# Kernel optimization log

Measured on AMD Instinct MI355X. Metric: run time of the kernel, lower is better.

## Reference

```python
import jax, jax.numpy as jnp
import numpy as np

N_NODES = 50000
N_EDGES = 1600000
IN_FEATS = 128
ENC_H = 20
DEC_H = 64


def setup_inputs() -> dict:
    key = jax.random.key(0)
    ks = jax.random.split(key, 14)
    inp = {}
    inp["x"] = jax.random.normal(ks[0], (N_NODES, IN_FEATS), dtype=jnp.float32)
    inp["edge_index"] = jax.random.randint(ks[1], (2, N_EDGES), 0, N_NODES, dtype=jnp.int64)
    inp["node_id"] = 0
    inp["noise_normal"] = jax.random.normal(ks[2], (N_EDGES, ENC_H), dtype=jnp.float32)
    inp["noise_u"] = jax.random.uniform(ks[3], (N_EDGES, 1), dtype=jnp.float32)
    # parameters (glorot-ish init)
    def lin(k, fan_in, fan_out):
        s = 1.0 / np.sqrt(fan_in)
        return jax.random.uniform(k, (fan_in, fan_out), jnp.float32, -s, s)
    inp["W_gc"] = lin(ks[4], IN_FEATS, ENC_H)
    inp["b_gc"] = jnp.zeros((ENC_H,), jnp.float32)
    inp["W_mu"] = lin(ks[5], 3 * ENC_H, ENC_H)
    inp["b_mu"] = jnp.zeros((ENC_H,), jnp.float32)
    inp["W_var"] = lin(ks[6], 3 * ENC_H, ENC_H)
    inp["b_var"] = jnp.zeros((ENC_H,), jnp.float32)
    inp["W_d1"] = lin(ks[7], ENC_H, DEC_H)
    inp["b_d1"] = jnp.zeros((DEC_H,), jnp.float32)
    inp["W_d2"] = lin(ks[8], DEC_H, 1)
    inp["b_d2"] = jnp.zeros((1,), jnp.float32)
    return inp


def _gcn_conv(x, edge_index, W, b):
    """PyG-style GCNConv: add self-loops, symmetric D^-1/2 (A+I) D^-1/2 norm."""
    n = x.shape[0]
    sl = jnp.arange(n, dtype=edge_index.dtype)
    row = jnp.concatenate([edge_index[0], sl])  # source
    col = jnp.concatenate([edge_index[1], sl])  # target
    xw = x @ W  # [N, H]
    deg = jax.ops.segment_sum(jnp.ones_like(col, dtype=xw.dtype), col, num_segments=n)
    dinv = jnp.where(deg > 0, jax.lax.rsqrt(deg), 0.0)
    norm = dinv[row] * dinv[col]  # [E+N]
    out = jax.ops.segment_sum(xw[row] * norm[:, None], col, num_segments=n)
    return out + b


def reference(x, edge_index, node_id, noise_normal, noise_u,
              W_gc, b_gc, W_mu, b_mu, W_var, b_var, W_d1, b_d1, W_d2, b_d2):
    # GCN encoder
    x1 = jax.nn.relu(_gcn_conv(x, edge_index, W_gc, b_gc))  # [N, H]
    # per-edge concat: [src_embed | dst_embed | node_id_embed]
    rows, cols = edge_index[0], edge_index[1]
    node_embed = jnp.broadcast_to(x1[node_id][None, :], (rows.shape[0], x1.shape[1]))
    x2 = jnp.concatenate([x1[rows], x1[cols], node_embed], axis=1)  # [E, 3H]
    # variational heads + reparameterization
    mu = x2 @ W_mu + b_mu
    sigma = jnp.exp(x2 @ W_var + b_var)
    z = mu + sigma * noise_normal  # [E, H]
    # decoder MLP
    h = jax.nn.relu(z @ W_d1 + b_d1)
    sampling_weights = jax.nn.relu(h @ W_d2 + b_d2)  # [E, 1]
    # gumbel-sigmoid sample (training=True, bias=0.0 -> bias'=1e-4, temperature=1.0)
    bias = 0.0001
    eps = (bias - (1.0 - bias)) * noise_u + (1.0 - bias)
    gate = jnp.log(eps) - jnp.log(1.0 - eps) + sampling_weights
    return jax.nn.sigmoid(gate)
```

## Files before the change

kernel.cpp:

```cpp
#include <hip/hip_runtime.h>

#define NFEAT 128
#define H 20
#define DH 64
#define SCAN_T 1024
#define BE 64
#define NB 192
#define HW 12800

typedef __attribute__((ext_vector_type(8))) short short8;
typedef __attribute__((ext_vector_type(4))) float f32x4;

__device__ __forceinline__ unsigned short f2bf(float f) {
    union { float f; unsigned u; } v; v.f = f;
    unsigned r = v.u + 0x7fff + ((v.u >> 16) & 1);
    return (unsigned short)(r >> 16);
}
__device__ __forceinline__ unsigned pk2(unsigned short a, unsigned short b) {
    return (unsigned)a | ((unsigned)b << 16);
}
__device__ __forceinline__ float bfel(uint4 v, int j) {
    unsigned word = (j < 2) ? v.x : (j < 4) ? v.y : (j < 6) ? v.z : v.w;
    unsigned u = (j & 1) ? (word & 0xFFFF0000u) : (word << 16);
    return __int_as_float((int)u);
}

template <int CTRL>
__device__ __forceinline__ float dpp_add(float x) {
    int y = __builtin_amdgcn_update_dpp(0, __float_as_int(x), CTRL, 0xF, 0xF, true);
    return x + __int_as_float(y);
}
__device__ __forceinline__ float sum16(float x) {
    x = dpp_add<0xB1>(x);
    x = dpp_add<0x4E>(x);
    x = dpp_add<0x124>(x);
    x = dpp_add<0x128>(x);
    return x;
}

__global__ __launch_bounds__(256) void k_prep(const float* __restrict__ Wd1,
                                              unsigned short* __restrict__ Bd1,
                                              int* __restrict__ deg, int* __restrict__ csum,
                                              float* __restrict__ bcat2, int N) {
    int t = blockIdx.x * blockDim.x + threadIdx.x;
    if (t < N) deg[t] = 0;
    if (t < 256) csum[t] = 0;
    if (t < 64) bcat2[t] = 0.f;
    if (t < 256) {
        int f = t >> 6, l = t & 63;
        int n = f * 16 + (l & 15);
#pragma unroll
        for (int j = 0; j < 8; j++) {
            int k = (l >> 4) * 8 + j;
            float v = (k < H) ? Wd1[k * DH + n] : 0.f;
            Bd1[(size_t)f * 512 + l * 8 + j] = f2bf(v);
        }
    }
}

__global__ __launch_bounds__(512) void k_hist(const int* __restrict__ cols,
                                              unsigned* __restrict__ hist, int* __restrict__ csum,
                                              int E, int N) {
    __shared__ unsigned h[HW];
    __shared__ int cs[256];
    int wstride = (N + 3) >> 2;
    int nchunks = (N + 255) >> 8;
    for (int i = threadIdx.x; i < wstride; i += 512) h[i] = 0;
    if (threadIdx.x < 256) cs[threadIdx.x] = 0;
    __syncthreads();
    int chunk = (E + NB - 1) / NB;
    int beg = blockIdx.x * chunk, end = min(beg + chunk, E);
    for (int i = beg + threadIdx.x; i < end; i += 512) {
        int c = __builtin_nontemporal_load(cols + i);
        atomicAdd(&h[c >> 2], 1u << ((c & 3) * 8));
    }
    __syncthreads();
    unsigned* dst = hist + (size_t)blockIdx.x * wstride;
    for (int i = threadIdx.x; i < wstride; i += 512) {
        unsigned w = h[i];
        dst[i] = w;
        if (w) {
            int s = (w & 0xFF) + ((w >> 8) & 0xFF) + ((w >> 16) & 0xFF) + (w >> 24);
            atomicAdd(&cs[i >> 6], s);
        }
    }
    __syncthreads();
    for (int j = threadIdx.x; j < nchunks; j += 512)
        if (cs[j]) atomicAdd(&csum[j], cs[j]);
}

__global__ __launch_bounds__(256) void k_scansmall(const int* __restrict__ chunkSum,
                                                   int* __restrict__ chunkOff, int nb) {
    __shared__ int sc[256];
    int t = threadIdx.x;
    int v0 = (t < nb) ? chunkSum[t] : 0;
    sc[t] = v0;
    __syncthreads();
    for (int off = 1; off < 256; off <<= 1) {
        int v = (t >= off) ? sc[t - off] : 0;
        __syncthreads();
        sc[t] += v;
        __syncthreads();
    }
    if (t < nb) chunkOff[t] = sc[t] - v0;
}

__global__ __launch_bounds__(256) void k_bases(const unsigned* __restrict__ hist,
                                               const int* __restrict__ chunkOff,
                                               unsigned char* __restrict__ delta,
                                               int* __restrict__ offsets, int* __restrict__ deg,
                                               int N, int E) {
    __shared__ int sc[256];
    int c = blockIdx.x * 256 + threadIdx.x;
    int wstride = (N + 3) >> 2;
    int sh = (c & 3) * 8;
    bool valid = c < N;
    int cw = valid ? (c >> 2) : 0;
    unsigned cnt[NB / 4];
    int d = 0;
#pragma unroll
    for (int b = 0; b < NB; b++) {
        unsigned w = hist[(size_t)b * wstride + cw];
        unsigned byte = (w >> sh) & 0xFF;
        if ((b & 3) == 0) cnt[b >> 2] = byte;
        else cnt[b >> 2] |= byte << ((b & 3) * 8);
        d += (int)byte;
    }
    if (!valid) d = 0;
    sc[threadIdx.x] = d;
    __syncthreads();
    for (int off = 1; off < 256; off <<= 1) {
        int v = (threadIdx.x >= off) ? sc[threadIdx.x - off] : 0;
        __syncthreads();
        sc[threadIdx.x] += v;
        __syncthreads();
    }
    if (valid) {
        int base = chunkOff[blockIdx.x] + sc[threadIdx.x] - d;
        offsets[c] = base;
        deg[c] = d;
        int run = 0;
#pragma unroll
        for (int b = 0; b < NB; b++) {
            delta[(size_t)b * N + c] = (unsigned char)run;
            run += (int)((cnt[b >> 2] >> ((b & 3) * 8)) & 0xFF);
        }
    }
    if (blockIdx.x == 0 && threadIdx.x == 0) offsets[N] = E;
}

__global__ __launch_bounds__(512) void k_place(const int* __restrict__ rows, const int* __restrict__ cols,
                                               const int* __restrict__ offsets,
                                               const unsigned char* __restrict__ delta,
                                               unsigned short* __restrict__ srcs, int E, int N) {
    __shared__ unsigned h[HW];
    int wstride = (N + 3) >> 2;
    for (int i = threadIdx.x; i < wstride; i += 512) h[i] = 0;
    __syncthreads();
    int chunk = (E + NB - 1) / NB;
    int beg = blockIdx.x * chunk, end = min(beg + chunk, E);
    const unsigned char* mydelta = delta + (size_t)blockIdx.x * N;
    for (int i = beg + threadIdx.x; i < end; i += 512) {
        int c = __builtin_nontemporal_load(cols + i);
        int r = __builtin_nontemporal_load(rows + i);
        int sh = (c & 3) * 8;
        unsigned old = atomicAdd(&h[c >> 2], 1u << sh);
        int rank = (old >> sh) & 0xFF;
        int pos = offsets[c] + (int)mydelta[c] + rank;
        srcs[pos] = (unsigned short)r;
    }
}

__global__ __launch_bounds__(256) void k_deg(const int* __restrict__ cols, int* __restrict__ deg, int E) {
    int t = blockIdx.x * blockDim.x + threadIdx.x;
    if (t < E) atomicAdd(&deg[cols[t]], 1);
}

__global__ __launch_bounds__(SCAN_T) void k_scan(const int* __restrict__ deg, int* __restrict__ offsets,
                                                 int* __restrict__ cursor, int N) {
    __shared__ int sums[SCAN_T];
    int t = threadIdx.x;
    int chunk = (N + SCAN_T - 1) / SCAN_T;
    int beg = t * chunk;
    int end = min(beg + chunk, N);
    int s = 0;
    for (int i = beg; i < end; i++) s += deg[i];
    sums[t] = s;
    __syncthreads();
    for (int off = 1; off < SCAN_T; off <<= 1) {
        int v = (t >= off) ? sums[t - off] : 0;
        __syncthreads();
        sums[t] += v;
        __syncthreads();
    }
    int run = (t == 0) ? 0 : sums[t - 1];
    for (int i = beg; i < end; i++) {
        offsets[i] = run;
        cursor[i] = run;
        run += deg[i];
    }
    if (t == SCAN_T - 1) offsets[N] = sums[SCAN_T - 1];
}

__global__ __launch_bounds__(256) void k_bucket_csr(const int* __restrict__ rows, const int* __restrict__ cols,
                                                    int* __restrict__ cursor, int* __restrict__ srcs, int E) {
    int e = blockIdx.x * blockDim.x + threadIdx.x;
    if (e >= E) return;
    int pos = atomicAdd(&cursor[cols[e]], 1);
    srcs[pos] = rows[e];
}

__global__ __launch_bounds__(256) void k_xw_xs(const float* __restrict__ x, const float* __restrict__ Wgc,
                                               const int* __restrict__ deg,
                                               float* __restrict__ xs, int N) {
    __shared__ float Ws[NFEAT * H];
    for (int i = threadIdx.x; i < NFEAT * H; i += blockDim.x) Ws[i] = Wgc[i];
    __syncthreads();
    int n = blockIdx.x * blockDim.x + threadIdx.x;
    if (n >= N) return;
    float acc[H];
#pragma unroll
    for (int j = 0; j < H; j++) acc[j] = 0.f;
    const float4* x4 = (const float4*)(x + (size_t)n * NFEAT);
#pragma unroll 4
    for (int k4 = 0; k4 < NFEAT / 4; k4++) {
        float4 xv = x4[k4];
#pragma unroll
        for (int s = 0; s < 4; s++) {
            float xk = (s == 0) ? xv.x : (s == 1) ? xv.y : (s == 2) ? xv.z : xv.w;
            const float4* wrow = (const float4*)(Ws + (k4 * 4 + s) * H);
#pragma unroll
            for (int q = 0; q < 5; q++) {
                float4 w = wrow[q];
                acc[q * 4 + 0] += xk * w.x;
                acc[q * 4 + 1] += xk * w.y;
                acc[q * 4 + 2] += xk * w.z;
                acc[q * 4 + 3] += xk * w.w;
            }
        }
    }
    float di = rsqrtf((float)(deg[n] + 1));
    float4* o = (float4*)(xs + (size_t)n * H);
#pragma unroll
    for (int q = 0; q < 5; q++)
        o[q] = make_float4(acc[q * 4 + 0] * di, acc[q * 4 + 1] * di, acc[q * 4 + 2] * di, acc[q * 4 + 3] * di);
}

template <typename IT>
__device__ __forceinline__ void gather_core16(const float* __restrict__ xs, const IT* __restrict__ idx,
                                              int beg, int end, int n, int sl, int degn,
                                              const float* __restrict__ bgc,
                                              unsigned short* __restrict__ PAo, unsigned short* __restrict__ PBo,
                                              int nid, const float* __restrict__ Wmu, const float* __restrict__ Wvar,
                                              const float* __restrict__ bmu, const float* __restrict__ bvar,
                                              float* __restrict__ bcat2) {
    float acc[H];
    if (sl == 0) {
        const float4* self = (const float4*)(xs + (size_t)n * H);
#pragma unroll
        for (int q = 0; q < 5; q++) {
            float4 v = self[q];
            acc[q * 4 + 0] = v.x; acc[q * 4 + 1] = v.y; acc[q * 4 + 2] = v.z; acc[q * 4 + 3] = v.w;
        }
    } else {
#pragma unroll
        for (int j = 0; j < H; j++) acc[j] = 0.f;
    }
#pragma unroll 2
    for (int i = beg + sl; i < end; i += 16) {
        int r = (int)__builtin_nontemporal_load(idx + i);
        const float4* p = (const float4*)(xs + (size_t)r * H);
#pragma unroll
        for (int q = 0; q < 5; q++) {
            float4 v = p[q];
            acc[q * 4 + 0] += v.x; acc[q * 4 + 1] += v.y; acc[q * 4 + 2] += v.z; acc[q * 4 + 3] += v.w;
        }
    }
#pragma unroll
    for (int j = 0; j < H; j++) acc[j] = sum16(acc[j]);
    float di = rsqrtf((float)(degn + 1));
    float x1f[H];
#pragma unroll
    for (int j = 0; j < H; j++) x1f[j] = fmaxf(di * acc[j] + bgc[j], 0.f);

#pragma unroll
    for (int t = 0; t < 6; t++) {
        int v = sl + 16 * t;
        int part = v / 24;
        int j = v - part * 24;
        float s = 0.f;
        if (j < 20) {
            const float* W = (part & 1) ? Wvar : Wmu;
            int k0 = (part < 2) ? 0 : 20;
#pragma unroll
            for (int k = 0; k < H; k++) s += x1f[k] * W[(k0 + k) * H + j];
        }
        unsigned short* T = (part < 2) ? PAo : PBo;
        int off = (j >> 3) * 16 + (part & 1) * 8 + (j & 7);
        T[(size_t)n * 48 + off] = f2bf(s);
    }

    if (n == nid) {
#pragma unroll
        for (int base = 0; base < 48; base += 16) {
            int jj = base + sl;
            if (jj < 40) {
                bool ismu = jj < 20;
                int col = ismu ? jj : jj - 20;
                const float* W = ismu ? Wmu : Wvar;
                float s = ismu ? bmu[col] : bvar[col];
#pragma unroll
                for (int k = 0; k < H; k++) s += x1f[k] * W[(2 * H + k) * H + col];
                bcat2[jj] = s;
            }
        }
    }
}

__global__ __launch_bounds__(256) void k_gather_csr16(const float* __restrict__ xs, const unsigned short* __restrict__ srcs,
                                                      const int* __restrict__ offsets, const int* __restrict__ deg,
                                                      const float* __restrict__ bgc,
                                                      unsigned short* __restrict__ PAo, unsigned short* __restrict__ PBo,
                                                      const int* __restrict__ node_id,
                                                      const float* __restrict__ Wmu, const float* __restrict__ Wvar,
                                                      const float* __restrict__ bmu, const float* __restrict__ bvar,
                                                      float* __restrict__ bcat2, int N) {
    int wave = (blockIdx.x * 256 + threadIdx.x) >> 6;
    int lane = threadIdx.x & 63;
    int n = wave * 4 + (lane >> 4);
    if (n >= N) return;
    gather_core16(xs, srcs, offsets[n], offsets[n + 1], n, lane & 15, deg[n], bgc, PAo, PBo,
                  node_id[0], Wmu, Wvar, bmu, bvar, bcat2);
}

__global__ __launch_bounds__(256) void k_gather_csr(const float* __restrict__ xs, const int* __restrict__ srcs,
                                                    const int* __restrict__ offsets, const int* __restrict__ deg,
                                                    const float* __restrict__ bgc,
                                                    unsigned short* __restrict__ PAo, unsigned short* __restrict__ PBo,
                                                    const int* __restrict__ node_id,
                                                    const float* __restrict__ Wmu, const float* __restrict__ Wvar,
                                                    const float* __restrict__ bmu, const float* __restrict__ bvar,
                                                    float* __restrict__ bcat2, int N) {
    int wave = (blockIdx.x * 256 + threadIdx.x) >> 6;
    int lane = threadIdx.x & 63;
    int n = wave * 4 + (lane >> 4);
    if (n >= N) return;
    gather_core16(xs, srcs, offsets[n], offsets[n + 1], n, lane & 15, deg[n], bgc, PAo, PBo,
                  node_id[0], Wmu, Wvar, bmu, bvar, bcat2);
}

__global__ __launch_bounds__(256) void k_mlp(
    const unsigned short* __restrict__ PA, const unsigned short* __restrict__ PBt,
    const int* __restrict__ rows, const int* __restrict__ cols,
    const float* __restrict__ noise_n, const float* __restrict__ noise_u,
    const unsigned short* __restrict__ Bd1g,
    const float* __restrict__ bcat2, const float* __restrict__ b_d1,
    const float* __restrict__ W_d2, const float* __restrict__ b_d2,
    float* __restrict__ out, int E) {

    int tid = threadIdx.x;
    int e0 = blockIdx.x * BE;
    int l = tid & 63, w = tid >> 6;
    int m = l & 15, quad = l >> 4;

    int ea = e0 + w * 16 + m;
    int ec = (ea < E) ? ea : E - 1;
    int r = rows[ec], c = cols[ec];

    uint4 pam = {0, 0, 0, 0}, pav = {0, 0, 0, 0}, pbm = {0, 0, 0, 0}, pbv = {0, 0, 0, 0};
    float nz[8], bm[8], bv[8];
#pragma unroll
    for (int j = 0; j < 8; j++) { nz[j] = 0.f; bm[j] = 0.f; bv[j] = 0.f; }
    if (quad < 3) {
        const char* pa = (const char*)PA + (size_t)r * 96 + quad * 32;
        const char* pb = (const char*)PBt + (size_t)c * 96 + quad * 32;
        pam = *(const uint4*)pa;  pav = *(const uint4*)(pa + 16);
        pbm = *(const uint4*)pb;  pbv = *(const uint4*)(pb + 16);
        float4 b0 = *(const float4*)(bcat2 + quad * 8);
        float4 b1 = *(const float4*)(bcat2 + quad * 8 + 4);
        bm[0] = b0.x; bm[1] = b0.y; bm[2] = b0.z; bm[3] = b0.w;
        bm[4] = b1.x; bm[5] = b1.y; bm[6] = b1.z; bm[7] = b1.w;
        float4 v0 = *(const float4*)(bcat2 + 20 + quad * 8);
        float4 v1 = *(const float4*)(bcat2 + 20 + quad * 8 + 4);
        bv[0] = v0.x; bv[1] = v0.y; bv[2] = v0.z; bv[3] = v0.w;
        bv[4] = v1.x; bv[5] = v1.y; bv[6] = v1.z; bv[7] = v1.w;
        const float* np = noise_n + (size_t)ec * H + quad * 8;
        float4 n0 = *(const float4*)np;
        nz[0] = n0.x; nz[1] = n0.y; nz[2] = n0.z; nz[3] = n0.w;
        if (quad < 2) {
            float4 n1 = *(const float4*)(np + 4);
            nz[4] = n1.x; nz[5] = n1.y; nz[6] = n1.z; nz[7] = n1.w;
        }
    }

    unsigned zp[4];
#pragma unroll
    for (int jj = 0; jj < 4; jj++) {
        unsigned short zh[2];
#pragma unroll
        for (int h2 = 0; h2 < 2; h2++) {
            int j = jj * 2 + h2;
            float zmu = bfel(pam, j) + bfel(pbm, j) + bm[j];
            float zva = bfel(pav, j) + bfel(pbv, j) + bv[j];
            float z = zmu + __expf(zva) * nz[j];
            z = (quad * 8 + j < 20) ? z : 0.f;
            zh[h2] = f2bf(z);
        }
        zp[jj] = pk2(zh[0], zh[1]);
    }
    union { unsigned u[4]; short8 s; } au;
    au.u[0] = zp[0]; au.u[1] = zp[1]; au.u[2] = zp[2]; au.u[3] = zp[3];
    short8 a2 = au.s;

    float p0 = 0.f, p1 = 0.f, p2 = 0.f, p3 = 0.f;
#pragma unroll
    for (int t4 = 0; t4 < 4; t4++) {
        f32x4 acc = {0.f, 0.f, 0.f, 0.f};
        short8 bb = *(const short8*)(Bd1g + t4 * 512 + l * 8);
        acc = __builtin_amdgcn_mfma_f32_16x16x32_bf16(a2, bb, acc, 0, 0, 0);
        int col = t4 * 16 + m;
        float bias = b_d1[col], wo = W_d2[col];
        p0 += fmaxf(acc[0] + bias, 0.f) * wo;
        p1 += fmaxf(acc[1] + bias, 0.f) * wo;
        p2 += fmaxf(acc[2] + bias, 0.f) * wo;
        p3 += fmaxf(acc[3] + bias, 0.f) * wo;
    }
    p0 = sum16(p0); p1 = sum16(p1); p2 = sum16(p2); p3 = sum16(p3);
    if (m < 4) {
        float swv = (m == 0) ? p0 : (m == 1) ? p1 : (m == 2) ? p2 : p3;
        int e = e0 + w * 16 + quad * 4 + m;
        if (e < E) {
            float sw = fmaxf(swv + b_d2[0], 0.f);
            float u = noise_u[e];
            float ev = 0.9999f - 0.9998f * u;
            float t = __expf(-sw);
            out[e] = ev / (ev + (1.f - ev) * t);
        }
    }
}

extern "C" void kernel_launch(void* const* d_in, const int* in_sizes, int n_in,
                              void* d_out, int out_size, void* d_ws, size_t ws_size,
                              hipStream_t stream) {
    const int N = in_sizes[0] / NFEAT;
    const int E = in_sizes[1] / 2;

    const float* x       = (const float*)d_in[0];
    const int*   ei      = (const int*)d_in[1];
    const int*   rows    = ei;
    const int*   cols    = ei + E;
    const int*   node_id = (const int*)d_in[2];
    const float* noise_n = (const float*)d_in[3];
    const float* noise_u = (const float*)d_in[4];
    const float* Wgc  = (const float*)d_in[5];
    const float* bgc  = (const float*)d_in[6];
    const float* Wmu  = (const float*)d_in[7];
    const float* bmu  = (const float*)d_in[8];
    const float* Wvar = (const float*)d_in[9];
    const float* bvar = (const float*)d_in[10];
    const float* Wd1  = (const float*)d_in[11];
    const float* bd1  = (const float*)d_in[12];
    const float* Wd2  = (const float*)d_in[13];
    const float* bd2  = (const float*)d_in[14];
    float* out = (float*)d_out;

    const int B = 256;
    int gN  = (N + B - 1) / B;
    int gG  = (N + 15) / 16;
    int gE  = (E + B - 1) / B;
    int gM  = (E + BE - 1) / BE;
    int nBins = (N + 255) / 256;

    char* ws = (char*)d_ws;
    size_t wstride   = (size_t)((N + 3) >> 2);
    size_t pa_sz     = (((size_t)N * 96) + 255) & ~255ULL;
    size_t hist_sz   = ((NB * wstride * 4) + 255) & ~255ULL;
    size_t histreg   = (hist_sz > 2 * pa_sz) ? hist_sz : 2 * pa_sz;
    size_t o_deg     = 0;
    size_t o_off     = o_deg  + (((size_t)N * 4 + 255) & ~255ULL);
    size_t o_csum    = o_off  + (((size_t)(N + 1) * 4 + 255) & ~255ULL);
    size_t o_coff    = o_csum + 1024;
    size_t o_hist    = o_coff + 1024;
    size_t o_delta   = o_hist  + histreg;
    size_t o_srcs    = o_delta + (((size_t)NB * N + 255) & ~255ULL);
    size_t o_xs      = o_srcs  + (((size_t)E * 2 + 255) & ~255ULL);
    size_t o_Bd1     = o_xs    + (((size_t)N * H * 4 + 255) & ~255ULL);
    size_t o_bcat2   = o_Bd1   + 4096;
    size_t need      = o_bcat2 + 256;

    bool main_path = (ws_size >= need) && (N <= 4 * HW) && (N < 65536) && (nBins <= 256);

    if (main_path) {
        int*   deg     = (int*)(ws + o_deg);
        int*   offsets = (int*)(ws + o_off);
        int*   csum    = (int*)(ws + o_csum);
        int*   coff    = (int*)(ws + o_coff);
        unsigned* hist = (unsigned*)(ws + o_hist);
        unsigned short* PA = (unsigned short*)(ws + o_hist);
        unsigned short* PB = (unsigned short*)(ws + o_hist + pa_sz);
        unsigned char* delta = (unsigned char*)(ws + o_delta);
        unsigned short* srcs = (unsigned short*)(ws + o_srcs);
        float* xs      = (float*)(ws + o_xs);
        unsigned short* Bd1  = (unsigned short*)(ws + o_Bd1);
        float* bcat2   = (float*)(ws + o_bcat2);

        k_prep<<<gN, B, 0, stream>>>(Wd1, Bd1, deg, csum, bcat2, N);
        k_hist<<<NB, 512, 0, stream>>>(cols, hist, csum, E, N);
        k_scansmall<<<1, B, 0, stream>>>(csum, coff, nBins);
        k_bases<<<nBins, B, 0, stream>>>(hist, coff, delta, offsets, deg, N, E);
        k_xw_xs<<<gN, B, 0, stream>>>(x, Wgc, deg, xs, N);
        k_place<<<NB, 512, 0, stream>>>(rows, cols, offsets, delta, srcs, E, N);
        k_gather_csr16<<<gG, B, 0, stream>>>(xs, srcs, offsets, deg, bgc, PA, PB,
                                             node_id, Wmu, Wvar, bmu, bvar, bcat2, N);
        k_mlp<<<gM, B, 0, stream>>>(PA, PB, rows, cols, noise_n, noise_u,
                                    Bd1, bcat2, bd1, Wd2, bd2, out, E);
    } else {
        size_t f_deg   = 0;
        size_t f_off   = f_deg + (((size_t)N * 4 + 255) & ~255ULL);
        size_t f_cur   = f_off + (((size_t)(N + 1) * 4 + 255) & ~255ULL);
        size_t f_srcs  = f_cur + (((size_t)N * 4 + 255) & ~255ULL);
        size_t f_xs    = f_srcs + (((size_t)E * 4 + 255) & ~255ULL);
        size_t f_PA    = f_xs + (((size_t)N * H * 4 + 255) & ~255ULL);
        size_t f_PB    = f_PA + pa_sz;
        size_t f_Bd1   = f_PB + pa_sz;
        size_t f_bcat2 = f_Bd1 + 4096;

        int*   deg     = (int*)(ws + f_deg);
        int*   offsets = (int*)(ws + f_off);
        int*   cursor  = (int*)(ws + f_cur);
        int*   srcs    = (int*)(ws + f_srcs);
        float* xs      = (float*)(ws + f_xs);
        unsigned short* PA = (unsigned short*)(ws + f_PA);
        unsigned short* PB = (unsigned short*)(ws + f_PB);
        unsigned short* Bd1 = (unsigned short*)(ws + f_Bd1);
        float* bcat2   = (float*)(ws + f_bcat2);

        k_prep<<<gN, B, 0, stream>>>(Wd1, Bd1, deg, cursor, bcat2, N);
        k_deg<<<gE, B, 0, stream>>>(cols, deg, E);
        k_scan<<<1, SCAN_T, 0, stream>>>(deg, offsets, cursor, N);
        k_bucket_csr<<<gE, B, 0, stream>>>(rows, cols, cursor, srcs, E);
        k_xw_xs<<<gN, B, 0, stream>>>(x, Wgc, deg, xs, N);
        k_gather_csr<<<gG, B, 0, stream>>>(xs, srcs, offsets, deg, bgc, PA, PB,
                                           node_id, Wmu, Wvar, bmu, bvar, bcat2, N);
        k_mlp<<<gM, B, 0, stream>>>(PA, PB, rows, cols, noise_n, noise_u,
                                    Bd1, bcat2, bd1, Wd2, bd2, out, E);
    }
}
```

Before: 431.2 us.

## Record ranks in histogram, flatten placement, compact PA/PB rows, two edge tiles per MLP wave

The histogram kernel now stores each edge's within-block rank, so the placement kernel becomes a flat one-thread-per-edge scatter and no longer needs a second LDS atomic pass with 192 large blocks. The per-node PA/PB bf16 rows shrink from 96 to 80 bytes by packing the last four mu/var features tightly, which cuts gather traffic in the MLP. The MLP kernel processes 128 edges per block, two 16-edge MFMA tiles per wave, to amortise bias and weight loads and raise memory-level parallelism. This costs an extra E-byte rank array write and read, plus more registers per thread in the MLP.

```diff
diff --git a/kernel.cpp b/kernel.cpp
--- a/kernel.cpp
+++ b/kernel.cpp
@@ -4,7 +4,7 @@
 #define H 20
 #define DH 64
 #define SCAN_T 1024
-#define BE 64
+#define BE2 128
 #define NB 192
 #define HW 12800
 
@@ -45,7 +45,7 @@
     int t = blockIdx.x * blockDim.x + threadIdx.x;
     if (t < N) deg[t] = 0;
     if (t < 256) csum[t] = 0;
-    if (t < 64) bcat2[t] = 0.f;
+    if (t < 128) bcat2[t] = 0.f;
     if (t < 256) {
         int f = t >> 6, l = t & 63;
         int n = f * 16 + (l & 15);
@@ -60,6 +60,7 @@
 
 __global__ __launch_bounds__(512) void k_hist(const int* __restrict__ cols,
                                               unsigned* __restrict__ hist, int* __restrict__ csum,
+                                              unsigned char* __restrict__ rank,
                                               int E, int N) {
     __shared__ unsigned h[HW];
     __shared__ int cs[256];
@@ -72,7 +73,9 @@
     int beg = blockIdx.x * chunk, end = min(beg + chunk, E);
     for (int i = beg + threadIdx.x; i < end; i += 512) {
         int c = __builtin_nontemporal_load(cols + i);
-        atomicAdd(&h[c >> 2], 1u << ((c & 3) * 8));
+        int sh = (c & 3) * 8;
+        unsigned old = atomicAdd(&h[c >> 2], 1u << sh);
+        rank[i] = (unsigned char)((old >> sh) & 0xFF);
     }
     __syncthreads();
     unsigned* dst = hist + (size_t)blockIdx.x * wstride;
@@ -149,26 +152,18 @@
     if (blockIdx.x == 0 && threadIdx.x == 0) offsets[N] = E;
 }
 
-__global__ __launch_bounds__(512) void k_place(const int* __restrict__ rows, const int* __restrict__ cols,
+__global__ __launch_bounds__(256) void k_place(const int* __restrict__ rows, const int* __restrict__ cols,
                                                const int* __restrict__ offsets,
                                                const unsigned char* __restrict__ delta,
-                                               unsigned short* __restrict__ srcs, int E, int N) {
-    __shared__ unsigned h[HW];
-    int wstride = (N + 3) >> 2;
-    for (int i = threadIdx.x; i < wstride; i += 512) h[i] = 0;
-    __syncthreads();
-    int chunk = (E + NB - 1) / NB;
-    int beg = blockIdx.x * chunk, end = min(beg + chunk, E);
-    const unsigned char* mydelta = delta + (size_t)blockIdx.x * N;
-    for (int i = beg + threadIdx.x; i < end; i += 512) {
-        int c = __builtin_nontemporal_load(cols + i);
-        int r = __builtin_nontemporal_load(rows + i);
-        int sh = (c & 3) * 8;
-        unsigned old = atomicAdd(&h[c >> 2], 1u << sh);
-        int rank = (old >> sh) & 0xFF;
-        int pos = offsets[c] + (int)mydelta[c] + rank;
-        srcs[pos] = (unsigned short)r;
-    }
+                                               const unsigned char* __restrict__ rank,
+                                               unsigned short* __restrict__ srcs, int E, int N, int chunk) {
+    int e = blockIdx.x * 256 + threadIdx.x;
+    if (e >= E) return;
+    int c = cols[e];
+    int r = rows[e];
+    int b = e / chunk;
+    int pos = offsets[c] + (int)delta[(size_t)b * N + c] + (int)rank[e];
+    srcs[pos] = (unsigned short)r;
 }
 
 __global__ __launch_bounds__(256) void k_deg(const int* __restrict__ cols, int* __restrict__ deg, int E) {
@@ -284,20 +279,19 @@
     for (int j = 0; j < H; j++) x1f[j] = fmaxf(di * acc[j] + bgc[j], 0.f);
 
 #pragma unroll
-    for (int t = 0; t < 6; t++) {
+    for (int t = 0; t < 5; t++) {
         int v = sl + 16 * t;
-        int part = v / 24;
-        int j = v - part * 24;
+        int part = v / 20;
+        int j = v - part * 20;
+        const float* W = (part & 1) ? Wvar : Wmu;
+        int k0 = (part < 2) ? 0 : 20;
         float s = 0.f;
-        if (j < 20) {
-            const float* W = (part & 1) ? Wvar : Wmu;
-            int k0 = (part < 2) ? 0 : 20;
-#pragma unroll
-            for (int k = 0; k < H; k++) s += x1f[k] * W[(k0 + k) * H + j];
-        }
+#pragma unroll
+        for (int k = 0; k < H; k++) s += x1f[k] * W[(k0 + k) * H + j];
         unsigned short* T = (part < 2) ? PAo : PBo;
-        int off = (j >> 3) * 16 + (part & 1) * 8 + (j & 7);
-        T[(size_t)n * 48 + off] = f2bf(s);
+        int off = (j < 16) ? ((j >> 3) * 16 + (part & 1) * 8 + (j & 7))
+                           : (32 + (part & 1) * 4 + (j - 16));
+        T[(size_t)n * 40 + off] = f2bf(s);
     }
 
     if (n == nid) {
@@ -311,7 +305,7 @@
                 float s = ismu ? bmu[col] : bvar[col];
 #pragma unroll
                 for (int k = 0; k < H; k++) s += x1f[k] * W[(2 * H + k) * H + col];
-                bcat2[jj] = s;
+                bcat2[ismu ? col : 64 + col] = s;
             }
         }
     }
@@ -349,6 +343,59 @@
                   node_id[0], Wmu, Wvar, bmu, bvar, bcat2);
 }
 
+__device__ __forceinline__ short8 build_a2(const unsigned short* __restrict__ PA,
+                                           const unsigned short* __restrict__ PBt,
+                                           const float* __restrict__ noise_n,
+                                           int em, int r, int c, int q,
+                                           const float (&bm)[8], const float (&bv)[8]) {
+    uint4 pam = {0, 0, 0, 0}, pav = pam, pbm = pam, pbv = pam;
+    float nz[8];
+#pragma unroll
+    for (int j = 0; j < 8; j++) nz[j] = 0.f;
+    if (q < 2) {
+        const char* pa = (const char*)PA + (size_t)r * 80 + q * 32;
+        const char* pb = (const char*)PBt + (size_t)c * 80 + q * 32;
+        pam = *(const uint4*)pa;  pav = *(const uint4*)(pa + 16);
+        pbm = *(const uint4*)pb;  pbv = *(const uint4*)(pb + 16);
+        const float* np = noise_n + (size_t)em * H + q * 8;
+        float4 n0 = *(const float4*)np;
+        float4 n1 = *(const float4*)(np + 4);
+        nz[0] = n0.x; nz[1] = n0.y; nz[2] = n0.z; nz[3] = n0.w;
+        nz[4] = n1.x; nz[5] = n1.y; nz[6] = n1.z; nz[7] = n1.w;
+    } else if (q == 2) {
+        const char* pa = (const char*)PA + (size_t)r * 80 + 64;
+        const char* pb = (const char*)PBt + (size_t)c * 80 + 64;
+        uint2 am = *(const uint2*)pa;
+        uint2 av = *(const uint2*)(pa + 8);
+        uint2 bm2 = *(const uint2*)pb;
+        uint2 bv2 = *(const uint2*)(pb + 8);
+        pam.x = am.x; pam.y = am.y;
+        pav.x = av.x; pav.y = av.y;
+        pbm.x = bm2.x; pbm.y = bm2.y;
+        pbv.x = bv2.x; pbv.y = bv2.y;
+        float4 n0 = *(const float4*)(noise_n + (size_t)em * H + 16);
+        nz[0] = n0.x; nz[1] = n0.y; nz[2] = n0.z; nz[3] = n0.w;
+    }
+    unsigned zp[4];
+#pragma unroll
+    for (int jj = 0; jj < 4; jj++) {
+        unsigned short zh[2];
+#pragma unroll
+        for (int h2 = 0; h2 < 2; h2++) {
+            int j = jj * 2 + h2;
+            float zmu = bfel(pam, j) + bfel(pbm, j) + bm[j];
+            float zva = bfel(pav, j) + bfel(pbv, j) + bv[j];
+            float z = zmu + __expf(zva) * nz[j];
+            z = (q * 8 + j < 20) ? z : 0.f;
+            zh[h2] = f2bf(z);
+        }
+        zp[jj] = pk2(zh[0], zh[1]);
+    }
+    union { unsigned u[4]; short8 s; } au;
+    au.u[0] = zp[0]; au.u[1] = zp[1]; au.u[2] = zp[2]; au.u[3] = zp[3];
+    return au.s;
+}
+
 __global__ __launch_bounds__(256) void k_mlp(
     const unsigned short* __restrict__ PA, const unsigned short* __restrict__ PBt,
     const int* __restrict__ rows, const int* __restrict__ cols,
@@ -359,82 +406,74 @@
     float* __restrict__ out, int E) {
 
     int tid = threadIdx.x;
-    int e0 = blockIdx.x * BE;
+    int e0 = blockIdx.x * BE2;
     int l = tid & 63, w = tid >> 6;
-    int m = l & 15, quad = l >> 4;
-
-    int ea = e0 + w * 16 + m;
-    int ec = (ea < E) ? ea : E - 1;
-    int r = rows[ec], c = cols[ec];
-
-    uint4 pam = {0, 0, 0, 0}, pav = {0, 0, 0, 0}, pbm = {0, 0, 0, 0}, pbv = {0, 0, 0, 0};
-    float nz[8], bm[8], bv[8];
-#pragma unroll
-    for (int j = 0; j < 8; j++) { nz[j] = 0.f; bm[j] = 0.f; bv[j] = 0.f; }
-    if (quad < 3) {
-        const char* pa = (const char*)PA + (size_t)r * 96 + quad * 32;
-        const char* pb = (const char*)PBt + (size_t)c * 96 + quad * 32;
-        pam = *(const uint4*)pa;  pav = *(const uint4*)(pa + 16);
-        pbm = *(const uint4*)pb;  pbv = *(const uint4*)(pb + 16);
-        float4 b0 = *(const float4*)(bcat2 + quad * 8);
-        float4 b1 = *(const float4*)(bcat2 + quad * 8 + 4);
+    int m = l & 15, q = l >> 4;
+
+    float bm[8], bv[8];
+#pragma unroll
+    for (int j = 0; j < 8; j++) { bm[j] = 0.f; bv[j] = 0.f; }
+    if (q < 3) {
+        float4 b0 = *(const float4*)(bcat2 + q * 8);
+        float4 b1 = *(const float4*)(bcat2 + q * 8 + 4);
         bm[0] = b0.x; bm[1] = b0.y; bm[2] = b0.z; bm[3] = b0.w;
         bm[4] = b1.x; bm[5] = b1.y; bm[6] = b1.z; bm[7] = b1.w;
-        float4 v0 = *(const float4*)(bcat2 + 20 + quad * 8);
-        float4 v1 = *(const float4*)(bcat2 + 20 + quad * 8 + 4);
+        float4 v0 = *(const float4*)(bcat2 + 64 + q * 8);
+        float4 v1 = *(const float4*)(bcat2 + 64 + q * 8 + 4);
         bv[0] = v0.x; bv[1] = v0.y; bv[2] = v0.z; bv[3] = v0.w;
         bv[4] = v1.x; bv[5] = v1.y; bv[6] = v1.z; bv[7] = v1.w;
-        const float* np = noise_n + (size_t)ec * H + quad * 8;
-        float4 n0 = *(const float4*)np;
-        nz[0] = n0.x; nz[1] = n0.y; nz[2] = n0.z; nz[3] = n0.w;
-        if (quad < 2) {
-            float4 n1 = *(const float4*)(np + 4);
-            nz[4] = n1.x; nz[5] = n1.y; nz[6] = n1.z; nz[7] = n1.w;
-        }
-    }
-
-    unsigned zp[4];
-#pragma unroll
-    for (int jj = 0; jj < 4; jj++) {
-        unsigned short zh[2];
-#pragma unroll
-        for (int h2 = 0; h2 < 2; h2++) {
-            int j = jj * 2 + h2;
-            float zmu = bfel(pam, j) + bfel(pbm, j) + bm[j];
-            float zva = bfel(pav, j) + bfel(pbv, j) + bv[j];
-            float z = zmu + __expf(zva) * nz[j];
-            z = (quad * 8 + j < 20) ? z : 0.f;
-            zh[h2] = f2bf(z);
-        }
-        zp[jj] = pk2(zh[0], zh[1]);
-    }
-    union { unsigned u[4]; short8 s; } au;
-    au.u[0] = zp[0]; au.u[1] = zp[1]; au.u[2] = zp[2]; au.u[3] = zp[3];
-    short8 a2 = au.s;
-
-    float p0 = 0.f, p1 = 0.f, p2 = 0.f, p3 = 0.f;
+    }
+
+    int ea0 = e0 + w * 16 + m;
+    int ea1 = ea0 + 64;
+    int em0 = (ea0 < E) ? ea0 : E - 1;
+    int em1 = (ea1 < E) ? ea1 : E - 1;
+    int r0 = rows[em0], c0 = cols[em0];
+    int r1 = rows[em1], c1 = cols[em1];
+
+    short8 a2_0 = (q < 3) ? build_a2(PA, PBt, noise_n, em0, r0, c0, q, bm, bv)
+                          : short8{0, 0, 0, 0, 0, 0, 0, 0};
+    short8 a2_1 = (q < 3) ? build_a2(PA, PBt, noise_n, em1, r1, c1, q, bm, bv)
+                          : short8{0, 0, 0, 0, 0, 0, 0, 0};
+
+    float p0a = 0.f, p1a = 0.f, p2a = 0.f, p3a = 0.f;
+    float p0b = 0.f, p1b = 0.f, p2b = 0.f, p3b = 0.f;
 #pragma unroll
     for (int t4 = 0; t4 < 4; t4++) {
-        f32x4 acc = {0.f, 0.f, 0.f, 0.f};
         short8 bb = *(const short8*)(Bd1g + t4 * 512 + l * 8);
-        acc = __builtin_amdgcn_mfma_f32_16x16x32_bf16(a2, bb, acc, 0, 0, 0);
+        f32x4 za = {0.f, 0.f, 0.f, 0.f};
+        f32x4 zb = {0.f, 0.f, 0.f, 0.f};
+        za = __builtin_amdgcn_mfma_f32_16x16x32_bf16(a2_0, bb, za, 0, 0, 0);
+        zb = __builtin_amdgcn_mfma_f32_16x16x32_bf16(a2_1, bb, zb, 0, 0, 0);
         int col = t4 * 16 + m;
         float bias = b_d1[col], wo = W_d2[col];
-        p0 += fmaxf(acc[0] + bias, 0.f) * wo;
-        p1 += fmaxf(acc[1] + bias, 0.f) * wo;
-        p2 += fmaxf(acc[2] + bias, 0.f) * wo;
-        p3 += fmaxf(acc[3] + bias, 0.f) * wo;
-    }
-    p0 = sum16(p0); p1 = sum16(p1); p2 = sum16(p2); p3 = sum16(p3);
+        p0a += fmaxf(za[0] + bias, 0.f) * wo;
+        p1a += fmaxf(za[1] + bias, 0.f) * wo;
+        p2a += fmaxf(za[2] + bias, 0.f) * wo;
+        p3a += fmaxf(za[3] + bias, 0.f) * wo;
+        p0b += fmaxf(zb[0] + bias, 0.f) * wo;
+        p1b += fmaxf(zb[1] + bias, 0.f) * wo;
+        p2b += fmaxf(zb[2] + bias, 0.f) * wo;
+        p3b += fmaxf(zb[3] + bias, 0.f) * wo;
+    }
+    p0a = sum16(p0a); p1a = sum16(p1a); p2a = sum16(p2a); p3a = sum16(p3a);
+    p0b = sum16(p0b); p1b = sum16(p1b); p2b = sum16(p2b); p3b = sum16(p3b);
     if (m < 4) {
-        float swv = (m == 0) ? p0 : (m == 1) ? p1 : (m == 2) ? p2 : p3;
-        int e = e0 + w * 16 + quad * 4 + m;
-        if (e < E) {
-            float sw = fmaxf(swv + b_d2[0], 0.f);
-            float u = noise_u[e];
+        float swa = (m == 0) ? p0a : (m == 1) ? p1a : (m == 2) ? p2a : p3a;
+        float swb = (m == 0) ? p0b : (m == 1) ? p1b : (m == 2) ? p2b : p3b;
+        int eA = e0 + w * 16 + q * 4 + m;
+        int eB = eA + 64;
+        if (eA < E) {
+            float sw = fmaxf(swa + b_d2[0], 0.f);
+            float u = noise_u[eA];
             float ev = 0.9999f - 0.9998f * u;
-            float t = __expf(-sw);
-            out[e] = ev / (ev + (1.f - ev) * t);
+            out[eA] = ev / (ev + (1.f - ev) * __expf(-sw));
+        }
+        if (eB < E) {
+            float sw = fmaxf(swb + b_d2[0], 0.f);
+            float u = noise_u[eB];
+            float ev = 0.9999f - 0.9998f * u;
+            out[eB] = ev / (ev + (1.f - ev) * __expf(-sw));
         }
     }
 }
@@ -468,12 +507,13 @@
     int gN  = (N + B - 1) / B;
     int gG  = (N + 15) / 16;
     int gE  = (E + B - 1) / B;
-    int gM  = (E + BE - 1) / BE;
+    int gM  = (E + BE2 - 1) / BE2;
     int nBins = (N + 255) / 256;
+    int chunk = (E + NB - 1) / NB;
 
     char* ws = (char*)d_ws;
     size_t wstride   = (size_t)((N + 3) >> 2);
-    size_t pa_sz     = (((size_t)N * 96) + 255) & ~255ULL;
+    size_t pa_sz     = (((size_t)N * 80) + 255) & ~255ULL;
     size_t hist_sz   = ((NB * wstride * 4) + 255) & ~255ULL;
     size_t histreg   = (hist_sz > 2 * pa_sz) ? hist_sz : 2 * pa_sz;
     size_t o_deg     = 0;
@@ -482,11 +522,12 @@
     size_t o_coff    = o_csum + 1024;
     size_t o_hist    = o_coff + 1024;
     size_t o_delta   = o_hist  + histreg;
-    size_t o_srcs    = o_delta + (((size_t)NB * N + 255) & ~255ULL);
+    size_t o_rank    = o_delta + (((size_t)NB * N + 255) & ~255ULL);
+    size_t o_srcs    = o_rank  + (((size_t)E + 255) & ~255ULL);
     size_t o_xs      = o_srcs  + (((size_t)E * 2 + 255) & ~255ULL);
     size_t o_Bd1     = o_xs    + (((size_t)N * H * 4 + 255) & ~255ULL);
     size_t o_bcat2   = o_Bd1   + 4096;
-    size_t need      = o_bcat2 + 256;
+    size_t need      = o_bcat2 + 512;
 
     bool main_path = (ws_size >= need) && (N <= 4 * HW) && (N < 65536) && (nBins <= 256);
 
@@ -499,17 +540,18 @@
         unsigned short* PA = (unsigned short*)(ws + o_hist);
         unsigned short* PB = (unsigned short*)(ws + o_hist + pa_sz);
         unsigned char* delta = (unsigned char*)(ws + o_delta);
+        unsigned char* rank  = (unsigned char*)(ws + o_rank);
         unsigned short* srcs = (unsigned short*)(ws + o_srcs);
         float* xs      = (float*)(ws + o_xs);
         unsigned short* Bd1  = (unsigned short*)(ws + o_Bd1);
         float* bcat2   = (float*)(ws + o_bcat2);
 
         k_prep<<<gN, B, 0, stream>>>(Wd1, Bd1, deg, csum, bcat2, N);
-        k_hist<<<NB, 512, 0, stream>>>(cols, hist, csum, E, N);
+        k_hist<<<NB, 512, 0, stream>>>(cols, hist, csum, rank, E, N);
         k_scansmall<<<1, B, 0, stream>>>(csum, coff, nBins);
         k_bases<<<nBins, B, 0, stream>>>(hist, coff, delta, offsets, deg, N, E);
         k_xw_xs<<<gN, B, 0, stream>>>(x, Wgc, deg, xs, N);
-        k_place<<<NB, 512, 0, stream>>>(rows, cols, offsets, delta, srcs, E, N);
+        k_place<<<gE, B, 0, stream>>>(rows, cols, offsets, delta, rank, srcs, E, N, chunk);
         k_gather_csr16<<<gG, B, 0, stream>>>(xs, srcs, offsets, deg, bgc, PA, PB,
                                              node_id, Wmu, Wvar, bmu, bvar, bcat2, N);
         k_mlp<<<gM, B, 0, stream>>>(PA, PB, rows, cols, noise_n, noise_u,
```

After: 443.8 us. 2.9% more time.
